# Kernel tuning notes

Hardware: AMD Instinct MI355X
Metric: run time of the kernel (lower is better)

The kernel has to match this reference:

```python
import jax, jax.numpy as jnp
import numpy as np

B, S, D, H = 4, 2048, 1024, 16
HD = D // H

def setup_inputs() -> dict:
    key = jax.random.key(0)
    ks = jax.random.split(key, 6)
    scale = 0.02
    return {
        "x": jax.random.normal(ks[0], (B, S, D), jnp.float32),
        "Wq": jax.random.normal(ks[1], (D, D), jnp.float32) * scale,
        "Wk": jax.random.normal(ks[2], (D, D), jnp.float32) * scale,
        "Wv": jax.random.normal(ks[3], (D, D), jnp.float32) * scale,
        "Wo": jax.random.normal(ks[4], (D, D), jnp.float32) * scale,
        "bo": jnp.zeros((D,), jnp.float32),
    }

def reference(x, Wq, Wk, Wv, Wo, bo):
    b, s, _ = x.shape
    # separate Q/K/V projections (no bias, qkv_bias=False)
    q = jnp.einsum('bsd,ed->bse', x, Wq).reshape(b, s, H, HD).transpose(0, 2, 1, 3)
    k = jnp.einsum('bsd,ed->bse', x, Wk).reshape(b, s, H, HD).transpose(0, 2, 1, 3)
    v = jnp.einsum('bsd,ed->bse', x, Wv).reshape(b, s, H, HD).transpose(0, 2, 1, 3)
    # full [B,H,S,S] scores, causal mask, scaled softmax (matches torch order:
    # mask applied to raw scores, then divide by sqrt(head_dim))
    scores = jnp.einsum('bhqd,bhkd->bhqk', q, k)
    causal = jnp.tril(jnp.ones((s, s), bool))
    scores = jnp.where(causal, scores, -jnp.inf)
    attn = jax.nn.softmax(scores / np.float32(np.sqrt(HD)), axis=-1)
    # dropout=0.0 -> identity in eval
    ctx = jnp.einsum('bhqk,bhkd->bhqd', attn, v)
    ctx = ctx.transpose(0, 2, 1, 3).reshape(b, s, D)
    return jnp.einsum('bsd,ed->bse', ctx, Wo) + bo
```

## Files before the change

kernel.cpp:

```cpp
#include <hip/hip_runtime.h>
#include <stdint.h>

#define DEVI __device__ __forceinline__

typedef __attribute__((ext_vector_type(8))) short bf16x8;
typedef __attribute__((ext_vector_type(8))) unsigned short u16x8;
typedef __attribute__((ext_vector_type(4))) float f32x4;
typedef unsigned short u16;
typedef unsigned int u32;

constexpr int B = 4, S = 2048, D = 1024, H = 16;
constexpr int BS = B * S;
constexpr int QS = 3 * D;
constexpr float CS = 0.18033688011112042f;

DEVI u16 f2bf(float f) {
  u32 u = __float_as_uint(f);
  u32 r = (u + 0x7FFFu + ((u >> 16) & 1u)) >> 16;
  return (u16)r;
}

DEVI void async_load16(const void* g, void* l) {
  __builtin_amdgcn_global_load_lds((const __attribute__((address_space(1))) u32*)g,
                                   (__attribute__((address_space(3))) u32*)l, 16, 0, 0);
}

__global__ void cast_f32_bf16(const float* __restrict__ in, u16* __restrict__ out, int n4) {
  int i = blockIdx.x * blockDim.x + threadIdx.x;
  if (i >= n4) return;
  float4 v = ((const float4*)in)[i];
  ushort4 o;
  o.x = f2bf(v.x); o.y = f2bf(v.y); o.z = f2bf(v.z); o.w = f2bf(v.w);
  ((ushort4*)out)[i] = o;
}

__global__ void cast_w4(const float* __restrict__ wq, const float* __restrict__ wk,
                        const float* __restrict__ wv, const float* __restrict__ wo,
                        u16* __restrict__ wqkv, u16* __restrict__ wob, int n4) {
  int i = blockIdx.x * blockDim.x + threadIdx.x;
  if (i >= n4) return;
  int y = blockIdx.y;
  const float* src = (y == 0) ? wq : (y == 1) ? wk : (y == 2) ? wv : wo;
  u16* dst = (y < 3) ? (wqkv + (size_t)y * D * D) : wob;
  float4 v = ((const float4*)src)[i];
  ushort4 o;
  o.x = f2bf(v.x); o.y = f2bf(v.y); o.z = f2bf(v.z); o.w = f2bf(v.w);
  ((ushort4*)dst)[i] = o;
}

template<int STORE_BF16, int ADD_BIAS, int SCALE_QCOLS>
__global__ __launch_bounds__(256)
void gemm_bt(const u16* __restrict__ A, const u16* __restrict__ Bt,
             const float* __restrict__ bias, void* __restrict__ Cout,
             int M, int N, int K) {
  __shared__ u16 a_lds[3][128 * 32];
  __shared__ u16 b_lds[3][128 * 32];
  const int tid = threadIdx.x, lane = tid & 63, wv = tid >> 6;
  const int m0 = blockIdx.x * 128, n0 = blockIdx.y * 128;
  const int wm = (wv >> 1) * 64, wn = (wv & 1) * 64;
  const int fr = lane & 15, fk = (lane >> 4) * 8;

  f32x4 acc[4][4] = {};

  const int seg = wv * 2;
  const int srow = seg * 16 + (lane >> 2);
  const int scolb = (lane & 3) * 16;
  const char* ab = (const char*)A + ((size_t)(m0 + srow) * K) * 2 + scolb;
  const char* bb = (const char*)Bt + ((size_t)(n0 + srow) * K) * 2 + scolb;
  const size_t row16 = (size_t)16 * K * 2;

  const int nsteps = K / 32;

  auto stage = [&](int bufid) {
    char* adst = (char*)a_lds[bufid] + seg * 1024;
    char* bdst = (char*)b_lds[bufid] + seg * 1024;
    async_load16(ab, adst);
    async_load16(ab + row16, adst + 1024);
    async_load16(bb, bdst);
    async_load16(bb + row16, bdst + 1024);
    ab += 64; bb += 64;
  };

  stage(0);
  if (nsteps > 1) stage(1);

  int cur = 0;
  for (int t = 0; t < nsteps; ++t) {
    if (t < nsteps - 1) asm volatile("s_waitcnt vmcnt(4)" ::: "memory");
    else                asm volatile("s_waitcnt vmcnt(0)" ::: "memory");
    asm volatile("s_barrier" ::: "memory");
    bf16x8 af[4], bfr[4];
    #pragma unroll
    for (int i = 0; i < 4; ++i) {
      af[i]  = *(const bf16x8*)&a_lds[cur][(wm + i * 16 + fr) * 32 + fk];
      bfr[i] = *(const bf16x8*)&b_lds[cur][(wn + i * 16 + fr) * 32 + fk];
    }
    if (t + 2 < nsteps) {
      int nxt = cur + 2; if (nxt >= 3) nxt -= 3;
      stage(nxt);
    }
    #pragma unroll
    for (int i = 0; i < 4; ++i)
      #pragma unroll
      for (int j = 0; j < 4; ++j)
        acc[i][j] = __builtin_amdgcn_mfma_f32_16x16x32_bf16(af[i], bfr[j], acc[i][j], 0, 0, 0);
    cur = (cur == 2) ? 0 : cur + 1;
  }

  const int cr = (lane >> 4) * 4, cc = lane & 15;
  const float qsc = (SCALE_QCOLS && n0 < 1024) ? CS : 1.0f;
  #pragma unroll
  for (int j = 0; j < 4; ++j) {
    int gn = n0 + wn + j * 16 + cc;
    float bv = ADD_BIAS ? bias[gn] : 0.0f;
    #pragma unroll
    for (int i = 0; i < 4; ++i) {
      #pragma unroll
      for (int r = 0; r < 4; ++r) {
        size_t idx = (size_t)(m0 + wm + i * 16 + cr + r) * N + gn;
        float v = acc[i][j][r];
        if (SCALE_QCOLS) v *= qsc;
        v += bv;
        if (STORE_BF16) ((u16*)Cout)[idx] = f2bf(v);
        else            ((float*)Cout)[idx] = v;
      }
    }
  }
}

__global__ __launch_bounds__(256, 4)
void attn_kernel(const u16* __restrict__ Q, const u16* __restrict__ K,
                 const u16* __restrict__ V, u16* __restrict__ C) {
  __shared__ u16 vt_lds[2][64 * 72];
  __shared__ u16 p_lds[4][16 * 72];

  const int tid = threadIdx.x, lane = tid & 63, wv = tid >> 6;
  const int f = blockIdx.x;
  const int pr = (f >> 3) & 15;
  const int g = (f & 7) | ((f >> 7) << 3);
  const int h = g & 15, b = g >> 4;

  const int fr = lane & 15, hi = lane >> 4, fk = hi * 8;
  const int cr = hi * 4, cc = fr;

  const size_t base = (size_t)(b * S) * QS + h * 64;
  const size_t cbase = (size_t)(b * S) * D + h * 64;

  const int vd0 = (tid & 7) * 8;
  const int vkvp = tid >> 3;
  const u16* Vg = V + base;
  const u16* Kg = K + base;

  int cur = 0;

  for (int half = 0; half < 2; ++half) {
    const int qt = half ? (31 - pr) : pr;
    const int q0 = qt * 64;
    const int qw = q0 + wv * 16;

    bf16x8 qf[2];
    {
      const u16* Qp = Q + base + (size_t)(qw + fr) * QS;
      #pragma unroll
      for (int kc = 0; kc < 2; ++kc)
        qf[kc] = *(const bf16x8*)(Qp + kc * 32 + fk);
    }

    f32x4 ctx[4] = {};
    float lr[4] = {};

    const int nt = qt + 1;

    u16x8 v0a, v0b, v1a, v1b;
    {
      const u16* vr = Vg + (size_t)(vkvp * 2) * QS + vd0;
      v0a = *(const u16x8*)vr;
      v0b = *(const u16x8*)(vr + QS);
    }

    for (int t = 0; t < nt; ++t) {
      const int kv0 = t * 64;
      const bool more = (t + 1 < nt);

      {
        #pragma unroll
        for (int i = 0; i < 8; ++i) {
          int d = vd0 + i;
          int kvp = vkvp ^ (((d >> 3) & 7) << 2);
          u32 w = (u32)(u16)v0a[i] | ((u32)(u16)v0b[i] << 16);
          *(u32*)&vt_lds[cur][d * 72 + kvp * 2] = w;
        }
      }

      bf16x8 kf[4][2];
      {
        const u16* kp = Kg + (size_t)(kv0 + fr) * QS + fk;
        #pragma unroll
        for (int ni = 0; ni < 4; ++ni)
          #pragma unroll
          for (int kc = 0; kc < 2; ++kc)
            kf[ni][kc] = *(const bf16x8*)(kp + (size_t)(ni * 16) * QS + kc * 32);
      }
      if (more) {
        const u16* vr = Vg + (size_t)((t + 1) * 64 + vkvp * 2) * QS + vd0;
        v1a = *(const u16x8*)vr;
        v1b = *(const u16x8*)(vr + QS);
      }

      asm volatile("s_waitcnt lgkmcnt(0)" ::: "memory");
      asm volatile("s_barrier" ::: "memory");

      f32x4 sc[4] = {};
      __builtin_amdgcn_s_setprio(1);
      #pragma unroll
      for (int ni = 0; ni < 4; ++ni)
        #pragma unroll
        for (int kc = 0; kc < 2; ++kc)
          sc[ni] = __builtin_amdgcn_mfma_f32_16x16x32_bf16(qf[kc], kf[ni][kc], sc[ni], 0, 0, 0);
      __builtin_amdgcn_s_setprio(0);

      if (t == nt - 1) {
        #pragma unroll
        for (int ni = 0; ni < 4; ++ni)
          #pragma unroll
          for (int r = 0; r < 4; ++r) {
            int qrow = qw + cr + r;
            int kvc = kv0 + ni * 16 + cc;
            if (kvc > qrow) sc[ni][r] = -3.0e38f;
          }
      }

      #pragma unroll
      for (int ni = 0; ni < 4; ++ni)
        #pragma unroll
        for (int r = 0; r < 4; ++r)
          sc[ni][r] = exp2f(sc[ni][r]);
      #pragma unroll
      for (int r = 0; r < 4; ++r) {
        float rs = (sc[0][r] + sc[1][r]) + (sc[2][r] + sc[3][r]);
        rs += __shfl_xor(rs, 1);
        rs += __shfl_xor(rs, 2);
        rs += __shfl_xor(rs, 4);
        rs += __shfl_xor(rs, 8);
        lr[r] += rs;
      }

      #pragma unroll
      for (int ni = 0; ni < 4; ++ni)
        #pragma unroll
        for (int r = 0; r < 4; ++r)
          p_lds[wv][(cr + r) * 72 + ni * 16 + cc] = f2bf(sc[ni][r]);

      asm volatile("s_waitcnt lgkmcnt(0)" ::: "memory");
      __builtin_amdgcn_sched_barrier(0);

      bf16x8 pa[2], vf[4][2];
      #pragma unroll
      for (int kc = 0; kc < 2; ++kc)
        pa[kc] = *(const bf16x8*)&p_lds[wv][fr * 72 + kc * 32 + fk];
      #pragma unroll
      for (int db = 0; db < 4; ++db)
        #pragma unroll
        for (int kc = 0; kc < 2; ++kc) {
          int d = db * 16 + fr;
          int kvp = (kc * 16 + hi * 4) ^ (((d >> 3) & 7) << 2);
          vf[db][kc] = *(const bf16x8*)&vt_lds[cur][d * 72 + kvp * 2];
        }
      __builtin_amdgcn_s_setprio(1);
      #pragma unroll
      for (int db = 0; db < 4; ++db)
        #pragma unroll
        for (int kc = 0; kc < 2; ++kc)
          ctx[db] = __builtin_amdgcn_mfma_f32_16x16x32_bf16(pa[kc], vf[db][kc], ctx[db], 0, 0, 0);
      __builtin_amdgcn_s_setprio(0);

      if (more) { v0a = v1a; v0b = v1b; }
      cur ^= 1;
    }

    u16* Cp = C + cbase + (size_t)qw * D;
    #pragma unroll
    for (int r = 0; r < 4; ++r) {
      float inv = 1.0f / lr[r];
      #pragma unroll
      for (int db = 0; db < 4; ++db)
        Cp[(size_t)(cr + r) * D + db * 16 + cc] = f2bf(ctx[db][r] * inv);
    }
  }
}

extern "C" void kernel_launch(void* const* d_in, const int* in_sizes, int n_in,
                              void* d_out, int out_size, void* d_ws, size_t ws_size,
                              hipStream_t stream) {
  const float* x  = (const float*)d_in[0];
  const float* Wq = (const float*)d_in[1];
  const float* Wk = (const float*)d_in[2];
  const float* Wv = (const float*)d_in[3];
  const float* Wo = (const float*)d_in[4];
  const float* bo = (const float*)d_in[5];

  char* ws = (char*)d_ws;
  u16* xb    = (u16*)(ws + 0);
  u16* Wqkvb = (u16*)(ws + (16u << 20));
  u16* Wob   = (u16*)(ws + (22u << 20));
  u16* QKVb  = (u16*)(ws + (24u << 20));
  u16* Cb    = (u16*)(ws + (72u << 20));

  const int XN = BS * D;
  const int WN = D * D;

  cast_f32_bf16<<<XN / 4 / 256, 256, 0, stream>>>(x, xb, XN / 4);
  cast_w4<<<dim3(WN / 4 / 256, 4), 256, 0, stream>>>(Wq, Wk, Wv, Wo, Wqkvb, Wob, WN / 4);

  gemm_bt<1, 0, 1><<<dim3(BS / 128, QS / 128), dim3(256), 0, stream>>>(xb, Wqkvb, nullptr, QKVb, BS, QS, D);

  attn_kernel<<<dim3(1024), dim3(256), 0, stream>>>(QKVb, QKVb + D, QKVb + 2 * D, Cb);

  gemm_bt<0, 1, 0><<<dim3(BS / 128, D / 128), dim3(256), 0, stream>>>(Cb, Wob, bo, d_out, BS, D, D);
}
```

Baseline: 323.2 us.

## Enlarge attention query tile to 128 rows with double-buffered K prefetch

The attention kernel now gives each wave 32 query rows (two 16-row MFMA tiles) instead of 16, so every K and V tile loaded is reused across twice as many queries, and the grid is halved. K fragments for the next tile are prefetched into a second register buffer while the current tile computes. The loop is unrolled by two through a macro, row-sum shuffles are deferred to the end, and tiles fully above the diagonal are skipped per wave. The cost is higher register pressure, with launch bounds relaxed to 2 blocks per CU, and fewer blocks to balance the causal workload.

Measured after the change: 271.2 us. -16.1%, faster.

```diff
diff --git a/kernel.cpp b/kernel.cpp
--- a/kernel.cpp
+++ b/kernel.cpp
@@ -128,16 +128,16 @@
   }
 }
 
-__global__ __launch_bounds__(256, 4)
+__global__ __launch_bounds__(256, 2)
 void attn_kernel(const u16* __restrict__ Q, const u16* __restrict__ K,
                  const u16* __restrict__ V, u16* __restrict__ C) {
   __shared__ u16 vt_lds[2][64 * 72];
-  __shared__ u16 p_lds[4][16 * 72];
+  __shared__ u16 p_lds[4][32 * 72];
 
   const int tid = threadIdx.x, lane = tid & 63, wv = tid >> 6;
   const int f = blockIdx.x;
-  const int pr = (f >> 3) & 15;
-  const int g = (f & 7) | ((f >> 7) << 3);
+  const int pair = (f >> 3) & 7;
+  const int g = (f & 7) | ((f >> 6) << 3);
   const int h = g & 15, b = g >> 4;
 
   const int fr = lane & 15, hi = lane >> 4, fk = hi * 8;
@@ -151,26 +151,130 @@
   const u16* Vg = V + base;
   const u16* Kg = K + base;
 
-  int cur = 0;
+#define LOAD_KF(KF, T)                                                         \
+  {                                                                            \
+    const u16* kp = Kg + (size_t)((T) * 64 + fr) * QS + fk;                    \
+    _Pragma("unroll")                                                          \
+    for (int ni = 0; ni < 4; ++ni)                                             \
+      _Pragma("unroll")                                                        \
+      for (int kc = 0; kc < 2; ++kc)                                           \
+        KF[ni][kc] = *(const bf16x8*)(kp + (size_t)(ni * 16) * QS + kc * 32);  \
+  }
+
+#define ATTN_TILE(T, BUF, VA, VB, VNA, VNB, KFC, KFN, PREF)                    \
+  {                                                                            \
+    const int kv0 = (T) * 64;                                                  \
+    _Pragma("unroll")                                                          \
+    for (int i = 0; i < 8; ++i) {                                              \
+      int d = vd0 + i;                                                         \
+      int kvp = vkvp ^ (((d >> 3) & 7) << 2);                                  \
+      u32 w = (u32)(u16)VA[i] | ((u32)(u16)VB[i] << 16);                       \
+      *(u32*)&vt_lds[BUF][d * 72 + kvp * 2] = w;                               \
+    }                                                                          \
+    if (PREF) {                                       \
+      const u16* vr = Vg + (size_t)(((T) + 1) * 64 + vkvp * 2) * QS + vd0;     \
+      VNA = *(const u16x8*)vr;                                                 \
+      VNB = *(const u16x8*)(vr + QS);                                          \
+    }                                                                          \
+    asm volatile("s_waitcnt lgkmcnt(0)" ::: "memory");                         \
+    asm volatile("s_barrier" ::: "memory");                                    \
+    if (kv0 <= qw + 31) {                                                      \
+      f32x4 sc[2][4] = {};                                                     \
+      __builtin_amdgcn_s_setprio(1);                                           \
+      _Pragma("unroll")                                                        \
+      for (int mi = 0; mi < 2; ++mi)                                           \
+        _Pragma("unroll")                                                      \
+        for (int ni = 0; ni < 4; ++ni)                                         \
+          _Pragma("unroll")                                                    \
+          for (int kc = 0; kc < 2; ++kc)                                       \
+            sc[mi][ni] = __builtin_amdgcn_mfma_f32_16x16x32_bf16(              \
+                qf[mi][kc], KFC[ni][kc], sc[mi][ni], 0, 0, 0);                 \
+      __builtin_amdgcn_s_setprio(0);                                           \
+      if ((PREF) && (((T) + 1) * 64 <= qw + 31)) LOAD_KF(KFN, (T) + 1)         \
+      if (kv0 + 63 > qw) {                                                     \
+        _Pragma("unroll")                                                      \
+        for (int mi = 0; mi < 2; ++mi)                                         \
+          _Pragma("unroll")                                                    \
+          for (int ni = 0; ni < 4; ++ni)                                       \
+            _Pragma("unroll")                                                  \
+            for (int r = 0; r < 4; ++r) {                                      \
+              int qrow = qw + mi * 16 + cr + r;                                \
+              int kvc = kv0 + ni * 16 + cc;                                    \
+              if (kvc > qrow) sc[mi][ni][r] = -3.0e38f;                        \
+            }                                                                  \
+      }                                                                        \
+      _Pragma("unroll")                                                        \
+      for (int mi = 0; mi < 2; ++mi)                                           \
+        _Pragma("unroll")                                                      \
+        for (int ni = 0; ni < 4; ++ni)                                         \
+          _Pragma("unroll")                                                    \
+          for (int r = 0; r < 4; ++r)                                          \
+            sc[mi][ni][r] = exp2f(sc[mi][ni][r]);                              \
+      _Pragma("unroll")                                                        \
+      for (int mi = 0; mi < 2; ++mi)                                           \
+        _Pragma("unroll")                                                      \
+        for (int r = 0; r < 4; ++r)                                            \
+          lrp[mi][r] += (sc[mi][0][r] + sc[mi][1][r]) +                        \
+                        (sc[mi][2][r] + sc[mi][3][r]);                         \
+      _Pragma("unroll")                                                        \
+      for (int mi = 0; mi < 2; ++mi)                                           \
+        _Pragma("unroll")                                                      \
+        for (int ni = 0; ni < 4; ++ni)                                         \
+          _Pragma("unroll")                                                    \
+          for (int r = 0; r < 4; ++r)                                          \
+            p_lds[wv][(mi * 16 + cr + r) * 72 + ni * 16 + cc] =                \
+                f2bf(sc[mi][ni][r]);                                           \
+           \
+      bf16x8 pa[2][2], vf[4][2];                                               \
+      _Pragma("unroll")                                                        \
+      for (int mi = 0; mi < 2; ++mi)                                           \
+        _Pragma("unroll")                                                      \
+        for (int kc = 0; kc < 2; ++kc)                                         \
+          pa[mi][kc] = *(const bf16x8*)&p_lds[wv][(mi * 16 + fr) * 72 +        \
+                                                  kc * 32 + fk];               \
+      _Pragma("unroll")                                                        \
+      for (int db = 0; db < 4; ++db)                                           \
+        _Pragma("unroll")                                                      \
+        for (int kc = 0; kc < 2; ++kc) {                                       \
+          int d = db * 16 + fr;                                                \
+          int kvp = (kc * 16 + hi * 4) ^ (((d >> 3) & 7) << 2);                \
+          vf[db][kc] = *(const bf16x8*)&vt_lds[BUF][d * 72 + kvp * 2];         \
+        }                                                                      \
+      __builtin_amdgcn_s_setprio(1);                                           \
+      _Pragma("unroll")                                                        \
+      for (int mi = 0; mi < 2; ++mi)                                           \
+        _Pragma("unroll")                                                      \
+        for (int db = 0; db < 4; ++db)                                         \
+          _Pragma("unroll")                                                    \
+          for (int kc = 0; kc < 2; ++kc)                                       \
+            ctx[mi][db] = __builtin_amdgcn_mfma_f32_16x16x32_bf16(             \
+                pa[mi][kc], vf[db][kc], ctx[mi][db], 0, 0, 0);                 \
+      __builtin_amdgcn_s_setprio(0);                                           \
+    }                                                                          \
+  }
 
   for (int half = 0; half < 2; ++half) {
-    const int qt = half ? (31 - pr) : pr;
-    const int q0 = qt * 64;
-    const int qw = q0 + wv * 16;
-
-    bf16x8 qf[2];
+    const int qt = half ? (15 - pair) : pair;
+    const int q0 = qt * 128;
+    const int qw = q0 + wv * 32;
+
+    bf16x8 qf[2][2];
     {
-      const u16* Qp = Q + base + (size_t)(qw + fr) * QS;
+      const u16* Qp = Q + base + (size_t)qw * QS;
       #pragma unroll
-      for (int kc = 0; kc < 2; ++kc)
-        qf[kc] = *(const bf16x8*)(Qp + kc * 32 + fk);
-    }
-
-    f32x4 ctx[4] = {};
-    float lr[4] = {};
-
-    const int nt = qt + 1;
-
+      for (int mi = 0; mi < 2; ++mi)
+        #pragma unroll
+        for (int kc = 0; kc < 2; ++kc)
+          qf[mi][kc] = *(const bf16x8*)(Qp + (size_t)(mi * 16 + fr) * QS + kc * 32 + fk);
+    }
+
+    f32x4 ctx[2][4] = {};
+    float lrp[2][4] = {};
+
+    const int nt = q0 / 64 + 2;
+
+    bf16x8 kfA[4][2], kfB[4][2];
+    LOAD_KF(kfA, 0)
     u16x8 v0a, v0b, v1a, v1b;
     {
       const u16* vr = Vg + (size_t)(vkvp * 2) * QS + vd0;
@@ -178,115 +282,29 @@
       v0b = *(const u16x8*)(vr + QS);
     }
 
-    for (int t = 0; t < nt; ++t) {
-      const int kv0 = t * 64;
-      const bool more = (t + 1 < nt);
-
-      {
-        #pragma unroll
-        for (int i = 0; i < 8; ++i) {
-          int d = vd0 + i;
-          int kvp = vkvp ^ (((d >> 3) & 7) << 2);
-          u32 w = (u32)(u16)v0a[i] | ((u32)(u16)v0b[i] << 16);
-          *(u32*)&vt_lds[cur][d * 72 + kvp * 2] = w;
-        }
-      }
-
-      bf16x8 kf[4][2];
-      {
-        const u16* kp = Kg + (size_t)(kv0 + fr) * QS + fk;
-        #pragma unroll
-        for (int ni = 0; ni < 4; ++ni)
-          #pragma unroll
-          for (int kc = 0; kc < 2; ++kc)
-            kf[ni][kc] = *(const bf16x8*)(kp + (size_t)(ni * 16) * QS + kc * 32);
-      }
-      if (more) {
-        const u16* vr = Vg + (size_t)((t + 1) * 64 + vkvp * 2) * QS + vd0;
-        v1a = *(const u16x8*)vr;
-        v1b = *(const u16x8*)(vr + QS);
-      }
-
-      asm volatile("s_waitcnt lgkmcnt(0)" ::: "memory");
-      asm volatile("s_barrier" ::: "memory");
-
-      f32x4 sc[4] = {};
-      __builtin_amdgcn_s_setprio(1);
-      #pragma unroll
-      for (int ni = 0; ni < 4; ++ni)
-        #pragma unroll
-        for (int kc = 0; kc < 2; ++kc)
-          sc[ni] = __builtin_amdgcn_mfma_f32_16x16x32_bf16(qf[kc], kf[ni][kc], sc[ni], 0, 0, 0);
-      __builtin_amdgcn_s_setprio(0);
-
-      if (t == nt - 1) {
-        #pragma unroll
-        for (int ni = 0; ni < 4; ++ni)
-          #pragma unroll
-          for (int r = 0; r < 4; ++r) {
-            int qrow = qw + cr + r;
-            int kvc = kv0 + ni * 16 + cc;
-            if (kvc > qrow) sc[ni][r] = -3.0e38f;
-          }
-      }
-
-      #pragma unroll
-      for (int ni = 0; ni < 4; ++ni)
-        #pragma unroll
-        for (int r = 0; r < 4; ++r)
-          sc[ni][r] = exp2f(sc[ni][r]);
+    for (int t = 0; t < nt; t += 2) {
+      ATTN_TILE(t,     0, v0a, v0b, v1a, v1b, kfA, kfB, true)
+      ATTN_TILE(t + 1, 1, v1a, v1b, v0a, v0b, kfB, kfA, (t + 2 < nt))
+    }
+
+    u16* Cp = C + cbase + (size_t)qw * D;
+    #pragma unroll
+    for (int mi = 0; mi < 2; ++mi)
       #pragma unroll
       for (int r = 0; r < 4; ++r) {
-        float rs = (sc[0][r] + sc[1][r]) + (sc[2][r] + sc[3][r]);
+        float rs = lrp[mi][r];
         rs += __shfl_xor(rs, 1);
         rs += __shfl_xor(rs, 2);
         rs += __shfl_xor(rs, 4);
         rs += __shfl_xor(rs, 8);
-        lr[r] += rs;
+        float inv = 1.0f / rs;
+        #pragma unroll
+        for (int db = 0; db < 4; ++db)
+          Cp[(size_t)(mi * 16 + cr + r) * D + db * 16 + cc] = f2bf(ctx[mi][db][r] * inv);
       }
-
-      #pragma unroll
-      for (int ni = 0; ni < 4; ++ni)
-        #pragma unroll
-        for (int r = 0; r < 4; ++r)
-          p_lds[wv][(cr + r) * 72 + ni * 16 + cc] = f2bf(sc[ni][r]);
-
-      asm volatile("s_waitcnt lgkmcnt(0)" ::: "memory");
-      __builtin_amdgcn_sched_barrier(0);
-
-      bf16x8 pa[2], vf[4][2];
-      #pragma unroll
-      for (int kc = 0; kc < 2; ++kc)
-        pa[kc] = *(const bf16x8*)&p_lds[wv][fr * 72 + kc * 32 + fk];
-      #pragma unroll
-      for (int db = 0; db < 4; ++db)
-        #pragma unroll
-        for (int kc = 0; kc < 2; ++kc) {
-          int d = db * 16 + fr;
-          int kvp = (kc * 16 + hi * 4) ^ (((d >> 3) & 7) << 2);
-          vf[db][kc] = *(const bf16x8*)&vt_lds[cur][d * 72 + kvp * 2];
-        }
-      __builtin_amdgcn_s_setprio(1);
-      #pragma unroll
-      for (int db = 0; db < 4; ++db)
-        #pragma unroll
-        for (int kc = 0; kc < 2; ++kc)
-          ctx[db] = __builtin_amdgcn_mfma_f32_16x16x32_bf16(pa[kc], vf[db][kc], ctx[db], 0, 0, 0);
-      __builtin_amdgcn_s_setprio(0);
-
-      if (more) { v0a = v1a; v0b = v1b; }
-      cur ^= 1;
-    }
-
-    u16* Cp = C + cbase + (size_t)qw * D;
-    #pragma unroll
-    for (int r = 0; r < 4; ++r) {
-      float inv = 1.0f / lr[r];
-      #pragma unroll
-      for (int db = 0; db < 4; ++db)
-        Cp[(size_t)(cr + r) * D + db * 16 + cc] = f2bf(ctx[db][r] * inv);
-    }
-  }
+  }
+#undef ATTN_TILE
+#undef LOAD_KF
 }
 
 extern "C" void kernel_launch(void* const* d_in, const int* in_sizes, int n_in,
@@ -314,7 +332,7 @@
 
   gemm_bt<1, 0, 1><<<dim3(BS / 128, QS / 128), dim3(256), 0, stream>>>(xb, Wqkvb, nullptr, QKVb, BS, QS, D);
 
-  attn_kernel<<<dim3(1024), dim3(256), 0, stream>>>(QKVb, QKVb + D, QKVb + 2 * D, Cb);
+  attn_kernel<<<dim3(512), dim3(256), 0, stream>>>(QKVb, QKVb + D, QKVb + 2 * D, Cb);
 
   gemm_bt<0, 1, 0><<<dim3(BS / 128, D / 128), dim3(256), 0, stream>>>(Cb, Wob, bo, d_out, BS, D, D);
 }
```
